# Performance work log

Measured on AMD Instinct MI355X. Metric: run time of the kernel, lower is better.

The kernel has to match this reference:

```python
import jax, jax.numpy as jnp
import numpy as np

EMBED_DIM = 768
NUM_HEADS = 12
HEAD_DIM = EMBED_DIM // NUM_HEADS
SCALING_FACTOR = 1.0
B, N = 1, 4096
K_PAIRS = 5


def setup_inputs() -> dict:
    key = jax.random.key(0)
    ks = jax.random.split(key, 10)
    s = EMBED_DIM ** -0.5
    return {
        "x": jax.random.normal(ks[0], (B, N, EMBED_DIM), dtype=jnp.float32),
        "similarity_matrix": jax.random.randint(ks[1], (N, K_PAIRS, 2), 0, N, dtype=jnp.int32),
        "Wq": jax.random.normal(ks[2], (EMBED_DIM, EMBED_DIM), dtype=jnp.float32) * s,
        "bq": jnp.zeros((EMBED_DIM,), dtype=jnp.float32),
        "Wk": jax.random.normal(ks[3], (EMBED_DIM, EMBED_DIM), dtype=jnp.float32) * s,
        "bk": jnp.zeros((EMBED_DIM,), dtype=jnp.float32),
        "Wv": jax.random.normal(ks[4], (EMBED_DIM, EMBED_DIM), dtype=jnp.float32) * s,
        "bv": jnp.zeros((EMBED_DIM,), dtype=jnp.float32),
        "Wo": jax.random.normal(ks[5], (EMBED_DIM, EMBED_DIM), dtype=jnp.float32) * s,
        "bo": jnp.zeros((EMBED_DIM,), dtype=jnp.float32),
    }


def _bias_matrix(similarity_matrix, n):
    # similarity_matrix: (N, K, 2) -> scatter-add SCALING_FACTOR at (i, idx)
    # for BOTH columns of every pair (duplicates accumulate, like +=).
    idx = similarity_matrix.reshape(n, -1)                 # (N, 2K)
    rows = jnp.broadcast_to(jnp.arange(n)[:, None], idx.shape)
    vals = jnp.where(idx < n, SCALING_FACTOR, 0.0).astype(jnp.float32)
    safe_idx = jnp.minimum(idx, n - 1)
    return jnp.zeros((n, n), dtype=jnp.float32).at[rows, safe_idx].add(vals)


def reference(x, similarity_matrix, Wq, bq, Wk, bk, Wv, bv, Wo, bo):
    b, n, c = x.shape
    h, d = NUM_HEADS, HEAD_DIM
    q = (x @ Wq.T + bq).reshape(b, n, h, d)
    k = (x @ Wk.T + bk).reshape(b, n, h, d)
    v = (x @ Wv.T + bv).reshape(b, n, h, d)
    scores = jnp.einsum("bihd,bjhd->bhij", q, k) * (d ** -0.5)  # (B,H,N,N)
    scores = scores + _bias_matrix(similarity_matrix, n)[None, None, :, :]
    attn = jax.nn.softmax(scores, axis=-1)
    out = jnp.einsum("bhij,bjhd->bihd", attn, v).reshape(b, n, c)
    return out @ Wo.T + bo
```

## Files before the change

kernel.cpp:

```cpp
#include <hip/hip_runtime.h>
#include <hip/hip_bf16.h>
#include <stdint.h>

#define N_TOK 4096
#define CDIM 768
#define NH 12
#define HD 64
#define SX (N_TOK * CDIM)
#define SW (CDIM * CDIM)

typedef __attribute__((ext_vector_type(8))) short bf16x8;
typedef __attribute__((ext_vector_type(4))) float f32x4;
typedef __attribute__((ext_vector_type(16))) float f32x16;
typedef unsigned short ushort_t;
typedef unsigned int uint_t;

typedef const __attribute__((address_space(1))) void* as1_cvp;
typedef __attribute__((address_space(3))) void* as3_vp;
#define GLD16(g, s) __builtin_amdgcn_global_load_lds((as1_cvp)(g), (as3_vp)(s), 16, 0, 0)

__device__ inline ushort_t f2bf(float f) {
    union { float f; uint_t u; } c; c.f = f;
    uint_t u = (c.u + 0x7FFFu + ((c.u >> 16) & 1u)) >> 16;
    return (ushort_t)u;
}
__device__ inline uint_t pack_bf2(float a, float b) {
    union { __hip_bfloat162 v; uint_t u; } c;
    c.v = __float22bfloat162_rn(make_float2(a, b));
    return c.u;
}

__global__ __launch_bounds__(256) void convert_all(
    const float* __restrict__ x,
    const float* __restrict__ Wq, const float* __restrict__ Wk,
    const float* __restrict__ Wv, const float* __restrict__ Wo,
    const float* __restrict__ bq, const float* __restrict__ bk, const float* __restrict__ bv,
    ushort_t* __restrict__ xb, ushort_t* __restrict__ Wf,
    ushort_t* __restrict__ Wob, float* __restrict__ biasf)
{
    long i = ((long)blockIdx.x * 256 + threadIdx.x) * 4;
    const float* src; ushort_t* dst; long off;
    if (i < SX)               { src = x;  dst = xb;          off = i; }
    else if (i < SX + SW)     { src = Wq; dst = Wf;          off = i - SX; }
    else if (i < SX + 2*SW)   { src = Wk; dst = Wf + SW;     off = i - SX - SW; }
    else if (i < SX + 3*SW)   { src = Wv; dst = Wf + 2*SW;   off = i - SX - 2*SW; }
    else if (i < SX + 4*SW)   { src = Wo; dst = Wob;         off = i - SX - 3*SW; }
    else if (i < SX + 4*SW + 3*CDIM) {
        long b = i - (SX + 4*SW);
        const float* bs = (b < CDIM) ? bq + b : (b < 2*CDIM) ? bk + (b - CDIM) : bv + (b - 2*CDIM);
        *(float4*)(biasf + b) = *(const float4*)bs;
        return;
    } else return;
    float4 v4 = *(const float4*)(src + off);
    uint2 st = { pack_bf2(v4.x, v4.y), pack_bf2(v4.z, v4.w) };
    *(uint2*)(dst + off) = st;
}

__global__ __launch_bounds__(256) void gemm_qkv(
    const ushort_t* __restrict__ xb, const ushort_t* __restrict__ Wf,
    const float* __restrict__ biasf,
    ushort_t* __restrict__ q, ushort_t* __restrict__ k, ushort_t* __restrict__ vT)
{
    __shared__ __align__(16) ushort_t Asm[128 * 64];
    __shared__ __align__(16) ushort_t Bsm[64 * 64];
    const int tid = threadIdx.x;
    const int w = tid >> 6, lane = tid & 63;
    const int quad = lane >> 4, l16 = lane & 15;
    const int row0 = blockIdx.x * 128;
    const int col0 = blockIdx.y * 64;
    const int rw = w * 32;
    const int srow = lane >> 3;
    const int sc = ((lane & 7) ^ srow) * 8;
    const int swz = l16 & 7;
    const float C1 = 0.18033688011112042f;

    f32x4 acc[2][4];
#pragma unroll
    for (int a = 0; a < 2; a++)
#pragma unroll
        for (int b = 0; b < 4; b++) acc[a][b] = (f32x4){0.f, 0.f, 0.f, 0.f};

    for (int kc = 0; kc < CDIM; kc += 64) {
        __syncthreads();
#pragma unroll
        for (int c = 0; c < 4; c++) {
            int ra = w * 32 + c * 8;
            GLD16(xb + (size_t)(row0 + ra + srow) * CDIM + kc + sc, &Asm[ra * 64]);
        }
#pragma unroll
        for (int c = 0; c < 2; c++) {
            int rb_ = w * 16 + c * 8;
            GLD16(Wf + (size_t)(col0 + rb_ + srow) * CDIM + kc + sc, &Bsm[rb_ * 64]);
        }
        __syncthreads();
#pragma unroll
        for (int kk = 0; kk < 2; kk++) {
            const int po = ((kk * 4 + quad) ^ swz) * 8;
            bf16x8 af[2], bfr[4];
#pragma unroll
            for (int rb = 0; rb < 2; rb++)
                af[rb] = *(const bf16x8*)&Asm[(rw + rb * 16 + l16) * 64 + po];
#pragma unroll
            for (int cb = 0; cb < 4; cb++)
                bfr[cb] = *(const bf16x8*)&Bsm[(cb * 16 + l16) * 64 + po];
#pragma unroll
            for (int rb = 0; rb < 2; rb++)
#pragma unroll
                for (int cb = 0; cb < 4; cb++)
                    acc[rb][cb] = __builtin_amdgcn_mfma_f32_16x16x32_bf16(af[rb], bfr[cb], acc[rb][cb], 0, 0, 0);
        }
    }

    if (col0 < 2 * CDIM) {
        const bool isQ = (col0 < CDIM);
        ushort_t* dst = isQ ? q : k;
        const int jb0 = isQ ? col0 : col0 - CDIM;
        const float scale = isQ ? C1 : 1.0f;
#pragma unroll
        for (int cb = 0; cb < 4; cb++) {
            int j = jb0 + cb * 16 + l16;
            float bv_ = biasf[col0 + cb * 16 + l16];
#pragma unroll
            for (int rb = 0; rb < 2; rb++)
#pragma unroll
                for (int r = 0; r < 4; r++) {
                    int i = row0 + rw + rb * 16 + quad * 4 + r;
                    dst[(size_t)i * CDIM + j] = f2bf((acc[rb][cb][r] + bv_) * scale);
                }
        }
    } else {
        const int jv0 = col0 - 2 * CDIM;
        ushort_t* T = Asm;
        __syncthreads();
#pragma unroll
        for (int cb = 0; cb < 4; cb++) {
            int jl = cb * 16 + l16;
            float bv_ = biasf[col0 + jl];
#pragma unroll
            for (int rb = 0; rb < 2; rb++)
#pragma unroll
                for (int r = 0; r < 4; r++) {
                    int i = rw + rb * 16 + quad * 4 + r;
                    T[jl * 128 + (((i >> 3) ^ (jl & 7)) * 8) + (i & 7)] =
                        f2bf(acc[rb][cb][r] + bv_);
                }
        }
        __syncthreads();
#pragma unroll
        for (int p = 0; p < 4; p++) {
            int t = tid + p * 256, jl = t >> 4, i8 = t & 15;
            *(bf16x8*)(vT + (size_t)(jv0 + jl) * N_TOK + row0 + i8 * 8) =
                *(const bf16x8*)&T[jl * 128 + ((i8 ^ (jl & 7)) * 8)];
        }
    }
}

__global__ __launch_bounds__(256) void gemm_out(
    const ushort_t* __restrict__ A, const ushort_t* __restrict__ W,
    const float* __restrict__ bias, float* __restrict__ out)
{
    __shared__ __align__(16) ushort_t Asm[64 * 64];
    __shared__ __align__(16) ushort_t Bsm[64 * 64];
    const int tid = threadIdx.x;
    const int w = tid >> 6, lane = tid & 63;
    const int quad = lane >> 4, l16 = lane & 15;
    const int row0 = blockIdx.x * 64;
    const int col0 = blockIdx.y * 64;
    const int srow = lane >> 3;
    const int sc = ((lane & 7) ^ srow) * 8;
    const int swz = l16 & 7;

    f32x4 acc[4];
#pragma unroll
    for (int b = 0; b < 4; b++) acc[b] = (f32x4){0.f, 0.f, 0.f, 0.f};

    for (int kc = 0; kc < CDIM; kc += 64) {
        __syncthreads();
#pragma unroll
        for (int c = 0; c < 2; c++) {
            int ra = w * 16 + c * 8;
            GLD16(A + (size_t)(row0 + ra + srow) * CDIM + kc + sc, &Asm[ra * 64]);
            GLD16(W + (size_t)(col0 + ra + srow) * CDIM + kc + sc, &Bsm[ra * 64]);
        }
        __syncthreads();
#pragma unroll
        for (int kk = 0; kk < 2; kk++) {
            const int po = ((kk * 4 + quad) ^ swz) * 8;
            bf16x8 af = *(const bf16x8*)&Asm[(w * 16 + l16) * 64 + po];
#pragma unroll
            for (int cb = 0; cb < 4; cb++) {
                bf16x8 bfr = *(const bf16x8*)&Bsm[(cb * 16 + l16) * 64 + po];
                acc[cb] = __builtin_amdgcn_mfma_f32_16x16x32_bf16(af, bfr, acc[cb], 0, 0, 0);
            }
        }
    }
#pragma unroll
    for (int cb = 0; cb < 4; cb++) {
        int j = col0 + cb * 16 + l16;
        float bv_ = bias[j];
#pragma unroll
        for (int r = 0; r < 4; r++) {
            int i = row0 + w * 16 + quad * 4 + r;
            out[(size_t)i * CDIM + j] = acc[cb][r] + bv_;
        }
    }
}

__global__ __launch_bounds__(256, 3) void attn_kernel(
    const ushort_t* __restrict__ Q, const ushort_t* __restrict__ K,
    const ushort_t* __restrict__ VT, const int* __restrict__ sim,
    ushort_t* __restrict__ Oout)
{
    __shared__ __align__(16) ushort_t smem[16384];
    __shared__ int ssim[64][12];
    __shared__ float psum[128];

    const int tid = threadIdx.x;
    const int w = tid >> 6, lane = tid & 63;
    const int hi = lane >> 5, l32 = lane & 31;
    const int qs = w >> 1, jh = w & 1;
    const float LOG2E = 1.4426950408889634f;

    const int lin = blockIdx.x;
    const int g = (lin & 7) * 96 + (lin >> 3);
    const int qbase = (g & 63) * 64;
    const int hoff = (g >> 6) * HD;

    const int srow = lane >> 3;
    const int sc = ((lane & 7) ^ srow) * 8;
    const ushort_t* kg0 = K + (size_t)(w * 16 + srow) * CDIM + hoff + sc;
    const ushort_t* kg1 = kg0 + 8 * CDIM;
    const ushort_t* vg0 = VT + (size_t)(hoff + w * 16 + srow) * N_TOK + sc;
    const ushort_t* vg1 = vg0 + 8 * (size_t)N_TOK;
    ushort_t* kda = &smem[(w * 16) * 64];
    ushort_t* vda = &smem[8192 + (w * 16) * 64];

#define STAGE(KD, VD) do { \
    GLD16(kg0, (KD)); GLD16(kg1, (KD) + 512); \
    GLD16(vg0, (VD)); GLD16(vg1, (VD) + 512); \
    kg0 += 64 * CDIM; kg1 += 64 * CDIM; vg0 += 64; vg1 += 64; } while (0)

    if (tid < 64) {
        int vb_[10];
        const int* sp = sim + (size_t)(qbase + tid) * 10;
#pragma unroll
        for (int e = 0; e < 10; e++) vb_[e] = sp[e];
#pragma unroll
        for (int round = 0; round < 10; round++)
#pragma unroll
            for (int i = (round & 1); i + 1 < 10; i += 2) {
                int a = vb_[i], b = vb_[i + 1];
                vb_[i] = min(a, b); vb_[i + 1] = max(a, b);
            }
#pragma unroll
        for (int e = 0; e < 10; e++) ssim[tid][e] = vb_[e];
        ssim[tid][10] = 0x7FFFFFFF;
        ssim[tid][11] = 0x7FFFFFFF;
    }

    bf16x8 qf[4];
    {
        const ushort_t* qp = Q + (size_t)(qbase + qs * 32 + l32) * CDIM + hoff + hi * 8;
#pragma unroll
        for (int kk = 0; kk < 4; kk++) qf[kk] = *(const bf16x8*)(qp + kk * 16);
    }

    const int swz = l32 & 7;
    const ushort_t* kfp[4];
#pragma unroll
    for (int kk = 0; kk < 4; kk++)
        kfp[kk] = &smem[(jh * 32 + l32) * 64 + (((kk * 2 + hi) ^ swz) * 8)];
    const ushort_t* vfp[2][2];
#pragma unroll
    for (int db = 0; db < 2; db++)
#pragma unroll
        for (int k2 = 0; k2 < 2; k2++)
            vfp[db][k2] = &smem[8192 + db * 2048 + l32 * 64 + (((jh * 4 + k2 * 2 + hi) ^ swz) * 8)];

    STAGE(kda, vda);
    __syncthreads();

    const int* srp = &ssim[qs * 32 + l32][0];
    int pt = 0, cu = srp[0];
    float lsum = 0.f;
    f32x16 Oacc0 = {0.f,0.f,0.f,0.f,0.f,0.f,0.f,0.f,0.f,0.f,0.f,0.f,0.f,0.f,0.f,0.f};
    f32x16 Oacc1 = {0.f,0.f,0.f,0.f,0.f,0.f,0.f,0.f,0.f,0.f,0.f,0.f,0.f,0.f,0.f,0.f};

#define TILE_BODY(OFS, J0) do { \
    f32x16 sacc = {0.f,0.f,0.f,0.f,0.f,0.f,0.f,0.f,0.f,0.f,0.f,0.f,0.f,0.f,0.f,0.f}; \
    _Pragma("unroll") \
    for (int kk = 0; kk < 4; kk++) { \
        bf16x8 kf = *(const bf16x8*)(kfp[kk] + (OFS)); \
        sacc = __builtin_amdgcn_mfma_f32_32x32x16_bf16(kf, qf[kk], sacc, 0, 0, 0); \
    } \
    { const int jend = (J0) + 64; \
      const int cb = (J0) + jh * 32 + hi * 4; \
      while (cu < jend) { \
        int d = cu - cb; \
        sacc[0]  += (d == 0)  ? LOG2E : 0.f; \
        sacc[1]  += (d == 1)  ? LOG2E : 0.f; \
        sacc[2]  += (d == 2)  ? LOG2E : 0.f; \
        sacc[3]  += (d == 3)  ? LOG2E : 0.f; \
        sacc[4]  += (d == 8)  ? LOG2E : 0.f; \
        sacc[5]  += (d == 9)  ? LOG2E : 0.f; \
        sacc[6]  += (d == 10) ? LOG2E : 0.f; \
        sacc[7]  += (d == 11) ? LOG2E : 0.f; \
        sacc[8]  += (d == 16) ? LOG2E : 0.f; \
        sacc[9]  += (d == 17) ? LOG2E : 0.f; \
        sacc[10] += (d == 18) ? LOG2E : 0.f; \
        sacc[11] += (d == 19) ? LOG2E : 0.f; \
        sacc[12] += (d == 24) ? LOG2E : 0.f; \
        sacc[13] += (d == 25) ? LOG2E : 0.f; \
        sacc[14] += (d == 26) ? LOG2E : 0.f; \
        sacc[15] += (d == 27) ? LOG2E : 0.f; \
        pt++; cu = srp[pt]; \
      } } \
    float e0  = __builtin_amdgcn_exp2f(sacc[0]); \
    float e1  = __builtin_amdgcn_exp2f(sacc[1]); \
    float e2  = __builtin_amdgcn_exp2f(sacc[2]); \
    float e3  = __builtin_amdgcn_exp2f(sacc[3]); \
    float e4  = __builtin_amdgcn_exp2f(sacc[4]); \
    float e5  = __builtin_amdgcn_exp2f(sacc[5]); \
    float e6  = __builtin_amdgcn_exp2f(sacc[6]); \
    float e7  = __builtin_amdgcn_exp2f(sacc[7]); \
    float e8  = __builtin_amdgcn_exp2f(sacc[8]); \
    float e9  = __builtin_amdgcn_exp2f(sacc[9]); \
    float e10 = __builtin_amdgcn_exp2f(sacc[10]); \
    float e11 = __builtin_amdgcn_exp2f(sacc[11]); \
    float e12 = __builtin_amdgcn_exp2f(sacc[12]); \
    float e13 = __builtin_amdgcn_exp2f(sacc[13]); \
    float e14 = __builtin_amdgcn_exp2f(sacc[14]); \
    float e15 = __builtin_amdgcn_exp2f(sacc[15]); \
    lsum += (((e0+e1)+(e2+e3)) + ((e4+e5)+(e6+e7))) \
          + (((e8+e9)+(e10+e11)) + ((e12+e13)+(e14+e15))); \
    uint_t A0 = pack_bf2(e0, e1),   C0 = pack_bf2(e2, e3); \
    uint_t B0 = pack_bf2(e4, e5),   D0 = pack_bf2(e6, e7); \
    uint_t A1 = pack_bf2(e8, e9),   C1_ = pack_bf2(e10, e11); \
    uint_t B1 = pack_bf2(e12, e13), D1 = pack_bf2(e14, e15); \
    asm("v_permlane32_swap_b32 %0, %1" : "+v"(A0), "+v"(B0)); \
    asm("v_permlane32_swap_b32 %0, %1" : "+v"(C0), "+v"(D0)); \
    asm("v_permlane32_swap_b32 %0, %1" : "+v"(A1), "+v"(B1)); \
    asm("v_permlane32_swap_b32 %0, %1" : "+v"(C1_), "+v"(D1)); \
    union { uint_t u[4]; bf16x8 v; } pa0_, pa1_; \
    pa0_.u[0] = A0; pa0_.u[1] = C0; pa0_.u[2] = B0; pa0_.u[3] = D0; \
    pa1_.u[0] = A1; pa1_.u[1] = C1_; pa1_.u[2] = B1; pa1_.u[3] = D1; \
    { \
        bf16x8 v00 = *(const bf16x8*)(vfp[0][0] + (OFS)); \
        bf16x8 v01 = *(const bf16x8*)(vfp[0][1] + (OFS)); \
        Oacc0 = __builtin_amdgcn_mfma_f32_32x32x16_bf16(pa0_.v, v00, Oacc0, 0, 0, 0); \
        Oacc0 = __builtin_amdgcn_mfma_f32_32x32x16_bf16(pa1_.v, v01, Oacc0, 0, 0, 0); \
        bf16x8 v10 = *(const bf16x8*)(vfp[1][0] + (OFS)); \
        bf16x8 v11 = *(const bf16x8*)(vfp[1][1] + (OFS)); \
        Oacc1 = __builtin_amdgcn_mfma_f32_32x32x16_bf16(pa0_.v, v10, Oacc1, 0, 0, 0); \
        Oacc1 = __builtin_amdgcn_mfma_f32_32x32x16_bf16(pa1_.v, v11, Oacc1, 0, 0, 0); \
    } \
  } while (0)

    for (int t = 0; t < 64; t += 2) {
        STAGE(kda + 4096, vda + 4096);
        TILE_BODY(0, t * 64);
        __syncthreads();
        if (t + 2 < 64) STAGE(kda, vda);
        TILE_BODY(4096, (t + 1) * 64);
        __syncthreads();
    }
#undef TILE_BODY
#undef STAGE

    float lt = lsum + __shfl_xor(lsum, 32, 64);
    if (lane < 32) psum[qs * 64 + jh * 32 + l32] = lt;

    float* Of = (float*)smem;
#define OROWS(OACC, DB, OP) do { \
    _Pragma("unroll") \
    for (int r = 0; r < 16; r++) { \
        int i_ = qs * 32 + (r & 3) + 8 * (r >> 2) + 4 * hi; \
        Of[i_ * 66 + (DB) * 32 + l32] OP (OACC)[r]; \
    } } while (0)

    if (jh == 0) { OROWS(Oacc0, 0, =); OROWS(Oacc1, 1, =); }
    __syncthreads();
    if (jh == 1) { OROWS(Oacc0, 0, +=); OROWS(Oacc1, 1, +=); }
    __syncthreads();
#undef OROWS

    {
        int row = tid >> 2, c0 = (tid & 3) * 16;
        int li = row & 31, qr = row >> 5;
        float inv = 1.0f / (psum[qr * 64 + li] + psum[qr * 64 + 32 + li]);
        const float* rp = Of + row * 66 + c0;
        uint_t w0 = pack_bf2(rp[0]  * inv, rp[1]  * inv);
        uint_t w1 = pack_bf2(rp[2]  * inv, rp[3]  * inv);
        uint_t w2 = pack_bf2(rp[4]  * inv, rp[5]  * inv);
        uint_t w3 = pack_bf2(rp[6]  * inv, rp[7]  * inv);
        uint_t w4 = pack_bf2(rp[8]  * inv, rp[9]  * inv);
        uint_t w5 = pack_bf2(rp[10] * inv, rp[11] * inv);
        uint_t w6 = pack_bf2(rp[12] * inv, rp[13] * inv);
        uint_t w7 = pack_bf2(rp[14] * inv, rp[15] * inv);
        union { uint_t u[4]; bf16x8 v; } oA, oB;
        oA.u[0] = w0; oA.u[1] = w1; oA.u[2] = w2; oA.u[3] = w3;
        oB.u[0] = w4; oB.u[1] = w5; oB.u[2] = w6; oB.u[3] = w7;
        ushort_t* op = Oout + (size_t)(qbase + row) * CDIM + hoff + c0;
        *(bf16x8*)op = oA.v;
        *(bf16x8*)(op + 8) = oB.v;
    }
}

extern "C" void kernel_launch(void* const* d_in, const int* in_sizes, int n_in,
                              void* d_out, int out_size, void* d_ws, size_t ws_size,
                              hipStream_t stream)
{
    const float* x   = (const float*)d_in[0];
    const int*   sim = (const int*)d_in[1];
    const float* Wq  = (const float*)d_in[2];
    const float* bq  = (const float*)d_in[3];
    const float* Wk  = (const float*)d_in[4];
    const float* bk  = (const float*)d_in[5];
    const float* Wv  = (const float*)d_in[6];
    const float* bv  = (const float*)d_in[7];
    const float* Wo  = (const float*)d_in[8];
    const float* bo  = (const float*)d_in[9];
    float* out = (float*)d_out;

    ushort_t* xb  = (ushort_t*)d_ws;
    ushort_t* q   = xb + SX;
    ushort_t* k   = q + SX;
    ushort_t* vT  = k + SX;
    ushort_t* Wf  = vT + SX;
    ushort_t* Wob = Wf + 3 * SW;
    float* biasf  = (float*)(Wob + SW);
    ushort_t* ao  = xb;

    dim3 blk(256);
    {
        long total4 = (long)(SX + 4 * SW + 3 * CDIM) / 4;
        int nb = (int)((total4 + 255) / 256);
        convert_all<<<nb, blk, 0, stream>>>(x, Wq, Wk, Wv, Wo, bq, bk, bv,
                                            xb, Wf, Wob, biasf);
    }
    {
        dim3 g(N_TOK / 128, (3 * CDIM) / 64);
        gemm_qkv<<<g, blk, 0, stream>>>(xb, Wf, biasf, q, k, vT);
    }
    {
        dim3 g((N_TOK / 64) * NH);
        attn_kernel<<<g, blk, 0, stream>>>(q, k, vT, sim, ao);
    }
    {
        dim3 g(N_TOK / 64, CDIM / 64);
        gemm_out<<<g, blk, 0, stream>>>(ao, Wob, bo, out);
    }
}
```

Before: 205.8 us.

## Software-pipeline QK^T of next tile with softmax and PV of current tile

Restructures the attention inner loop so the QK^T MFMAs for the next K/V tile are issued before the bias, exp and PV work of the current tile, using two score accumulators. V fragments are read from LDS into registers before each barrier so the buffer can be refilled earlier, and the prologue stages both buffers up front. MFMA sections are wrapped in s_setprio to favour matrix issue across waves. The cost is higher register pressure from a second score accumulator plus held V registers, which could lower occupancy, and the barrier and staging order becomes more fragile.

```diff
diff --git a/kernel.cpp b/kernel.cpp
--- a/kernel.cpp
+++ b/kernel.cpp
@@ -277,60 +277,69 @@
         for (int k2 = 0; k2 < 2; k2++)
             vfp[db][k2] = &smem[8192 + db * 2048 + l32 * 64 + (((jh * 4 + k2 * 2 + hi) ^ swz) * 8)];
 
-    STAGE(kda, vda);
-    __syncthreads();
-
     const int* srp = &ssim[qs * 32 + l32][0];
-    int pt = 0, cu = srp[0];
     float lsum = 0.f;
     f32x16 Oacc0 = {0.f,0.f,0.f,0.f,0.f,0.f,0.f,0.f,0.f,0.f,0.f,0.f,0.f,0.f,0.f,0.f};
     f32x16 Oacc1 = {0.f,0.f,0.f,0.f,0.f,0.f,0.f,0.f,0.f,0.f,0.f,0.f,0.f,0.f,0.f,0.f};
-
-#define TILE_BODY(OFS, J0) do { \
-    f32x16 sacc = {0.f,0.f,0.f,0.f,0.f,0.f,0.f,0.f,0.f,0.f,0.f,0.f,0.f,0.f,0.f,0.f}; \
+    f32x16 saccA, saccB;
+    bf16x8 vr00, vr01, vr10, vr11;
+
+#define S_TILE(OFS, DST) do { \
+    (DST) = (f32x16){0.f,0.f,0.f,0.f,0.f,0.f,0.f,0.f,0.f,0.f,0.f,0.f,0.f,0.f,0.f,0.f}; \
+    __builtin_amdgcn_s_setprio(1); \
     _Pragma("unroll") \
     for (int kk = 0; kk < 4; kk++) { \
         bf16x8 kf = *(const bf16x8*)(kfp[kk] + (OFS)); \
-        sacc = __builtin_amdgcn_mfma_f32_32x32x16_bf16(kf, qf[kk], sacc, 0, 0, 0); \
+        (DST) = __builtin_amdgcn_mfma_f32_32x32x16_bf16(kf, qf[kk], (DST), 0, 0, 0); \
     } \
+    __builtin_amdgcn_s_setprio(0); \
+  } while (0)
+
+#define VREAD(OFS) do { \
+    vr00 = *(const bf16x8*)(vfp[0][0] + (OFS)); \
+    vr01 = *(const bf16x8*)(vfp[0][1] + (OFS)); \
+    vr10 = *(const bf16x8*)(vfp[1][0] + (OFS)); \
+    vr11 = *(const bf16x8*)(vfp[1][1] + (OFS)); } while (0)
+
+#define SOFTPV(SACC, J0) do { \
     { const int jend = (J0) + 64; \
       const int cb = (J0) + jh * 32 + hi * 4; \
       while (cu < jend) { \
         int d = cu - cb; \
-        sacc[0]  += (d == 0)  ? LOG2E : 0.f; \
-        sacc[1]  += (d == 1)  ? LOG2E : 0.f; \
-        sacc[2]  += (d == 2)  ? LOG2E : 0.f; \
-        sacc[3]  += (d == 3)  ? LOG2E : 0.f; \
-        sacc[4]  += (d == 8)  ? LOG2E : 0.f; \
-        sacc[5]  += (d == 9)  ? LOG2E : 0.f; \
-        sacc[6]  += (d == 10) ? LOG2E : 0.f; \
-        sacc[7]  += (d == 11) ? LOG2E : 0.f; \
-        sacc[8]  += (d == 16) ? LOG2E : 0.f; \
-        sacc[9]  += (d == 17) ? LOG2E : 0.f; \
-        sacc[10] += (d == 18) ? LOG2E : 0.f; \
-        sacc[11] += (d == 19) ? LOG2E : 0.f; \
-        sacc[12] += (d == 24) ? LOG2E : 0.f; \
-        sacc[13] += (d == 25) ? LOG2E : 0.f; \
-        sacc[14] += (d == 26) ? LOG2E : 0.f; \
-        sacc[15] += (d == 27) ? LOG2E : 0.f; \
+        (SACC)[0]  += (d == 0)  ? LOG2E : 0.f; \
+        (SACC)[1]  += (d == 1)  ? LOG2E : 0.f; \
+        (SACC)[2]  += (d == 2)  ? LOG2E : 0.f; \
+        (SACC)[3]  += (d == 3)  ? LOG2E : 0.f; \
+        (SACC)[4]  += (d == 8)  ? LOG2E : 0.f; \
+        (SACC)[5]  += (d == 9)  ? LOG2E : 0.f; \
+        (SACC)[6]  += (d == 10) ? LOG2E : 0.f; \
+        (SACC)[7]  += (d == 11) ? LOG2E : 0.f; \
+        (SACC)[8]  += (d == 16) ? LOG2E : 0.f; \
+        (SACC)[9]  += (d == 17) ? LOG2E : 0.f; \
+        (SACC)[10] += (d == 18) ? LOG2E : 0.f; \
+        (SACC)[11] += (d == 19) ? LOG2E : 0.f; \
+        (SACC)[12] += (d == 24) ? LOG2E : 0.f; \
+        (SACC)[13] += (d == 25) ? LOG2E : 0.f; \
+        (SACC)[14] += (d == 26) ? LOG2E : 0.f; \
+        (SACC)[15] += (d == 27) ? LOG2E : 0.f; \
         pt++; cu = srp[pt]; \
       } } \
-    float e0  = __builtin_amdgcn_exp2f(sacc[0]); \
-    float e1  = __builtin_amdgcn_exp2f(sacc[1]); \
-    float e2  = __builtin_amdgcn_exp2f(sacc[2]); \
-    float e3  = __builtin_amdgcn_exp2f(sacc[3]); \
-    float e4  = __builtin_amdgcn_exp2f(sacc[4]); \
-    float e5  = __builtin_amdgcn_exp2f(sacc[5]); \
-    float e6  = __builtin_amdgcn_exp2f(sacc[6]); \
-    float e7  = __builtin_amdgcn_exp2f(sacc[7]); \
-    float e8  = __builtin_amdgcn_exp2f(sacc[8]); \
-    float e9  = __builtin_amdgcn_exp2f(sacc[9]); \
-    float e10 = __builtin_amdgcn_exp2f(sacc[10]); \
-    float e11 = __builtin_amdgcn_exp2f(sacc[11]); \
-    float e12 = __builtin_amdgcn_exp2f(sacc[12]); \
-    float e13 = __builtin_amdgcn_exp2f(sacc[13]); \
-    float e14 = __builtin_amdgcn_exp2f(sacc[14]); \
-    float e15 = __builtin_amdgcn_exp2f(sacc[15]); \
+    float e0  = __builtin_amdgcn_exp2f((SACC)[0]); \
+    float e1  = __builtin_amdgcn_exp2f((SACC)[1]); \
+    float e2  = __builtin_amdgcn_exp2f((SACC)[2]); \
+    float e3  = __builtin_amdgcn_exp2f((SACC)[3]); \
+    float e4  = __builtin_amdgcn_exp2f((SACC)[4]); \
+    float e5  = __builtin_amdgcn_exp2f((SACC)[5]); \
+    float e6  = __builtin_amdgcn_exp2f((SACC)[6]); \
+    float e7  = __builtin_amdgcn_exp2f((SACC)[7]); \
+    float e8  = __builtin_amdgcn_exp2f((SACC)[8]); \
+    float e9  = __builtin_amdgcn_exp2f((SACC)[9]); \
+    float e10 = __builtin_amdgcn_exp2f((SACC)[10]); \
+    float e11 = __builtin_amdgcn_exp2f((SACC)[11]); \
+    float e12 = __builtin_amdgcn_exp2f((SACC)[12]); \
+    float e13 = __builtin_amdgcn_exp2f((SACC)[13]); \
+    float e14 = __builtin_amdgcn_exp2f((SACC)[14]); \
+    float e15 = __builtin_amdgcn_exp2f((SACC)[15]); \
     lsum += (((e0+e1)+(e2+e3)) + ((e4+e5)+(e6+e7))) \
           + (((e8+e9)+(e10+e11)) + ((e12+e13)+(e14+e15))); \
     uint_t A0 = pack_bf2(e0, e1),   C0 = pack_bf2(e2, e3); \
@@ -344,27 +353,36 @@
     union { uint_t u[4]; bf16x8 v; } pa0_, pa1_; \
     pa0_.u[0] = A0; pa0_.u[1] = C0; pa0_.u[2] = B0; pa0_.u[3] = D0; \
     pa1_.u[0] = A1; pa1_.u[1] = C1_; pa1_.u[2] = B1; pa1_.u[3] = D1; \
-    { \
-        bf16x8 v00 = *(const bf16x8*)(vfp[0][0] + (OFS)); \
-        bf16x8 v01 = *(const bf16x8*)(vfp[0][1] + (OFS)); \
-        Oacc0 = __builtin_amdgcn_mfma_f32_32x32x16_bf16(pa0_.v, v00, Oacc0, 0, 0, 0); \
-        Oacc0 = __builtin_amdgcn_mfma_f32_32x32x16_bf16(pa1_.v, v01, Oacc0, 0, 0, 0); \
-        bf16x8 v10 = *(const bf16x8*)(vfp[1][0] + (OFS)); \
-        bf16x8 v11 = *(const bf16x8*)(vfp[1][1] + (OFS)); \
-        Oacc1 = __builtin_amdgcn_mfma_f32_32x32x16_bf16(pa0_.v, v10, Oacc1, 0, 0, 0); \
-        Oacc1 = __builtin_amdgcn_mfma_f32_32x32x16_bf16(pa1_.v, v11, Oacc1, 0, 0, 0); \
-    } \
+    __builtin_amdgcn_s_setprio(1); \
+    Oacc0 = __builtin_amdgcn_mfma_f32_32x32x16_bf16(pa0_.v, vr00, Oacc0, 0, 0, 0); \
+    Oacc0 = __builtin_amdgcn_mfma_f32_32x32x16_bf16(pa1_.v, vr01, Oacc0, 0, 0, 0); \
+    Oacc1 = __builtin_amdgcn_mfma_f32_32x32x16_bf16(pa0_.v, vr10, Oacc1, 0, 0, 0); \
+    Oacc1 = __builtin_amdgcn_mfma_f32_32x32x16_bf16(pa1_.v, vr11, Oacc1, 0, 0, 0); \
+    __builtin_amdgcn_s_setprio(0); \
   } while (0)
 
+    STAGE(kda, vda);
+    __syncthreads();
+    STAGE(kda + 4096, vda + 4096);
+
+    int pt = 0, cu = srp[0];
+    S_TILE(0, saccA);
+
     for (int t = 0; t < 64; t += 2) {
-        STAGE(kda + 4096, vda + 4096);
-        TILE_BODY(0, t * 64);
+        VREAD(0);
         __syncthreads();
         if (t + 2 < 64) STAGE(kda, vda);
-        TILE_BODY(4096, (t + 1) * 64);
-        __syncthreads();
-    }
-#undef TILE_BODY
+        S_TILE(4096, saccB);
+        SOFTPV(saccA, t * 64);
+        VREAD(4096);
+        __syncthreads();
+        if (t + 3 < 64) STAGE(kda + 4096, vda + 4096);
+        if (t + 2 < 64) S_TILE(0, saccA);
+        SOFTPV(saccB, (t + 1) * 64);
+    }
+#undef SOFTPV
+#undef VREAD
+#undef S_TILE
 #undef STAGE
 
     float lt = lsum + __shfl_xor(lsum, 32, 64);
```

Measured after the change: 213.9 us. 1.04x slower.

## Triple-buffer K/V tiles with vmcnt-based waits and MFMA priority hints

Applied to the files above, without the earlier changes.

Switches the attention kernel's K/V LDS staging from double to triple buffering, keeping two tiles in flight. Barriers now wait only on the oldest outstanding global-to-LDS loads via s_waitcnt vmcnt instead of draining everything. It also hoists the V fragment reads ahead of the PV MFMAs and wraps MFMA groups in s_setprio. LDS per block grows from 32KB to 48KB, which may cut the 3-blocks-per-CU occupancy, and the hand-counted vmcnt values must match the issued loads exactly.

```diff
diff --git a/kernel.cpp b/kernel.cpp
--- a/kernel.cpp
+++ b/kernel.cpp
@@ -211,8 +211,8 @@
     const ushort_t* __restrict__ VT, const int* __restrict__ sim,
     ushort_t* __restrict__ Oout)
 {
-    __shared__ __align__(16) ushort_t smem[16384];
-    __shared__ int ssim[64][12];
+    __shared__ __align__(16) ushort_t smem[24576];
+    __shared__ int ssim[64][13];
     __shared__ float psum[128];
 
     const int tid = threadIdx.x;
@@ -233,13 +233,20 @@
     const ushort_t* vg0 = VT + (size_t)(hoff + w * 16 + srow) * N_TOK + sc;
     const ushort_t* vg1 = vg0 + 8 * (size_t)N_TOK;
     ushort_t* kda = &smem[(w * 16) * 64];
-    ushort_t* vda = &smem[8192 + (w * 16) * 64];
+    ushort_t* vda = &smem[4096 + (w * 16) * 64];
 
 #define STAGE(KD, VD) do { \
     GLD16(kg0, (KD)); GLD16(kg1, (KD) + 512); \
     GLD16(vg0, (VD)); GLD16(vg1, (VD) + 512); \
     kg0 += 64 * CDIM; kg1 += 64 * CDIM; vg0 += 64; vg1 += 64; } while (0)
 
+#define SYNCV do { \
+    asm volatile("s_waitcnt vmcnt(4)" ::: "memory"); \
+    __builtin_amdgcn_s_barrier(); \
+    asm volatile("" ::: "memory"); \
+    __builtin_amdgcn_sched_barrier(0); \
+} while (0)
+
     if (tid < 64) {
         int vb_[10];
         const int* sp = sim + (size_t)(qbase + tid) * 10;
@@ -275,10 +282,17 @@
     for (int db = 0; db < 2; db++)
 #pragma unroll
         for (int k2 = 0; k2 < 2; k2++)
-            vfp[db][k2] = &smem[8192 + db * 2048 + l32 * 64 + (((jh * 4 + k2 * 2 + hi) ^ swz) * 8)];
+            vfp[db][k2] = &smem[4096 + db * 2048 + l32 * 64 + (((jh * 4 + k2 * 2 + hi) ^ swz) * 8)];
+
+    __syncthreads();
 
     STAGE(kda, vda);
-    __syncthreads();
+    STAGE(kda + 8192, vda + 8192);
+    STAGE(kda + 16384, vda + 16384);
+    asm volatile("s_waitcnt vmcnt(8)" ::: "memory");
+    __builtin_amdgcn_s_barrier();
+    asm volatile("" ::: "memory");
+    __builtin_amdgcn_sched_barrier(0);
 
     const int* srp = &ssim[qs * 32 + l32][0];
     int pt = 0, cu = srp[0];
@@ -288,11 +302,13 @@
 
 #define TILE_BODY(OFS, J0) do { \
     f32x16 sacc = {0.f,0.f,0.f,0.f,0.f,0.f,0.f,0.f,0.f,0.f,0.f,0.f,0.f,0.f,0.f,0.f}; \
+    __builtin_amdgcn_s_setprio(1); \
     _Pragma("unroll") \
     for (int kk = 0; kk < 4; kk++) { \
         bf16x8 kf = *(const bf16x8*)(kfp[kk] + (OFS)); \
         sacc = __builtin_amdgcn_mfma_f32_32x32x16_bf16(kf, qf[kk], sacc, 0, 0, 0); \
     } \
+    __builtin_amdgcn_s_setprio(0); \
     { const int jend = (J0) + 64; \
       const int cb = (J0) + jh * 32 + hi * 4; \
       while (cu < jend) { \
@@ -347,24 +363,38 @@
     { \
         bf16x8 v00 = *(const bf16x8*)(vfp[0][0] + (OFS)); \
         bf16x8 v01 = *(const bf16x8*)(vfp[0][1] + (OFS)); \
+        bf16x8 v10 = *(const bf16x8*)(vfp[1][0] + (OFS)); \
+        bf16x8 v11 = *(const bf16x8*)(vfp[1][1] + (OFS)); \
+        __builtin_amdgcn_s_setprio(1); \
         Oacc0 = __builtin_amdgcn_mfma_f32_32x32x16_bf16(pa0_.v, v00, Oacc0, 0, 0, 0); \
         Oacc0 = __builtin_amdgcn_mfma_f32_32x32x16_bf16(pa1_.v, v01, Oacc0, 0, 0, 0); \
-        bf16x8 v10 = *(const bf16x8*)(vfp[1][0] + (OFS)); \
-        bf16x8 v11 = *(const bf16x8*)(vfp[1][1] + (OFS)); \
         Oacc1 = __builtin_amdgcn_mfma_f32_32x32x16_bf16(pa0_.v, v10, Oacc1, 0, 0, 0); \
         Oacc1 = __builtin_amdgcn_mfma_f32_32x32x16_bf16(pa1_.v, v11, Oacc1, 0, 0, 0); \
+        __builtin_amdgcn_s_setprio(0); \
     } \
   } while (0)
 
-    for (int t = 0; t < 64; t += 2) {
-        STAGE(kda + 4096, vda + 4096);
-        TILE_BODY(0, t * 64);
-        __syncthreads();
-        if (t + 2 < 64) STAGE(kda, vda);
-        TILE_BODY(4096, (t + 1) * 64);
-        __syncthreads();
-    }
+    int j0 = 0;
+    for (int it = 0; it < 21; ++it) {
+        TILE_BODY(0, j0);
+        SYNCV;
+        STAGE(kda, vda);
+        TILE_BODY(8192, j0 + 64);
+        SYNCV;
+        if (it < 20) STAGE(kda + 8192, vda + 8192);
+        TILE_BODY(16384, j0 + 128);
+        SYNCV;
+        if (it < 20) STAGE(kda + 16384, vda + 16384);
+        j0 += 192;
+    }
+    asm volatile("s_waitcnt vmcnt(0)" ::: "memory");
+    __builtin_amdgcn_s_barrier();
+    asm volatile("" ::: "memory");
+    __builtin_amdgcn_sched_barrier(0);
+    TILE_BODY(0, 4032);
+    __syncthreads();
 #undef TILE_BODY
+#undef SYNCV
 #undef STAGE
 
     float lt = lsum + __shfl_xor(lsum, 32, 64);
```

Measured after the change: 210.1 us. 2.1% more time.
